# Performance work log

Measured on AMD Instinct MI355X. Metric: run time of the kernel, lower is better.

Reference implementation:

```python
import jax, jax.numpy as jnp
import numpy as np

EPS = 1e-9

def dice(x, alpha):
    # Dice: batch-norm over dim 0 (unbiased var, ddof=1), then gated blend.
    mu = jnp.mean(x, axis=0)
    var = jnp.var(x, axis=0, ddof=1)
    p = jax.nn.sigmoid((x - mu) / jnp.sqrt(var + EPS))
    return alpha * x * (1.0 - p) + x * p


def setup_inputs() -> dict:
    key = jax.random.key(0)
    ks = jax.random.split(key, 8)
    bs, seq, dim = 2048, 200, 64
    d_in = dim * 4
    return {
        "query": jax.random.normal(ks[0], (bs, dim), jnp.float32),
        "user_behavior": jax.random.normal(ks[1], (bs, seq, dim), jnp.float32),
        "mask": jax.random.uniform(ks[2], (bs, seq, 1), jnp.float32),
        "W1": jax.random.normal(ks[3], (d_in, 32), jnp.float32) / np.sqrt(d_in),
        "b1": jnp.zeros((32,), jnp.float32),
        "alpha1": jnp.zeros((1,), jnp.float32),
        "W2": jax.random.normal(ks[4], (32, 16), jnp.float32) / np.sqrt(32.0),
        "b2": jnp.zeros((16,), jnp.float32),
        "alpha2": jnp.zeros((1,), jnp.float32),
        "W3": jax.random.normal(ks[5], (16, 1), jnp.float32) / np.sqrt(16.0),
        "b3": jnp.zeros((1,), jnp.float32),
    }


def reference(query, user_behavior, mask, W1, b1, alpha1, W2, b2, alpha2, W3, b3):
    # query: (bs, dim) -> broadcast to (bs, seq, dim)
    q = jnp.broadcast_to(query[:, None, :], user_behavior.shape)
    attn_input = jnp.concatenate(
        [q, user_behavior, q - user_behavior, q * user_behavior], axis=-1
    )  # (bs, seq, 4*dim)
    h = dice(attn_input @ W1 + b1, alpha1)
    h = dice(h @ W2 + b2, alpha2)
    attns = h @ W3 + b3  # (bs, seq, 1)
    attns = attns * mask
    output = jnp.sum(user_behavior * attns, axis=1)  # (bs, dim)
    return output, attns
```

## Files before the change

### kernel.cpp

```cpp
#include <hip/hip_runtime.h>
#include <math.h>

#define BS  2048
#define SEQ 200
#define DIM 64
#define C1  32
#define C2  16
#define PAD 68

__device__ __forceinline__ float dice1(float x, float m, float r, float al) {
    float t = (x - m) * r;
    float p = 1.f / (1.f + __expf(-t));
    return x * (al + p * (1.f - al));
}

__global__ __launch_bounds__(256) void k_gemm1(const float* __restrict__ q,
                                               const float* __restrict__ ub,
                                               const float* __restrict__ W1,
                                               const float* __restrict__ b1,
                                               float* __restrict__ z1) {
    const int bs = blockIdx.x;
    const int tid = threadIdx.x;
    __shared__ __align__(16) float s_ub[SEQ * PAD];
    __shared__ __align__(16) float s_wc[DIM * C1];
    __shared__ __align__(16) float s_qw[C1];

    float4* s_ub4 = (float4*)s_ub;
    const float4* s_wc4 = (const float4*)s_wc;
    const float* qrow = q + bs * DIM;
    const float* ub_b = ub + (size_t)bs * SEQ * DIM;

    const float4* src4 = (const float4*)ub_b;
    for (int t = tid; t < SEQ * 16; t += 256)
        s_ub4[(t >> 4) * 17 + (t & 15)] = src4[t];

    const float4* w1b4 = (const float4*)(W1 + DIM * C1);
    const float4* w1c4 = (const float4*)(W1 + 2 * DIM * C1);
    const float4* w1d4 = (const float4*)(W1 + 3 * DIM * C1);
    for (int i4 = tid; i4 < DIM * C1 / 4; i4 += 256) {
        int d = i4 >> 3;
        float qd = qrow[d];
        float4 bb = w1b4[i4], cc = w1c4[i4], dd = w1d4[i4];
        float4 r;
        r.x = bb.x - cc.x + qd * dd.x;
        r.y = bb.y - cc.y + qd * dd.y;
        r.z = bb.z - cc.z + qd * dd.z;
        r.w = bb.w - cc.w + qd * dd.w;
        ((float4*)s_wc)[i4] = r;
    }
    if (tid < C1) {
        float a = b1[tid];
        #pragma unroll 8
        for (int d = 0; d < DIM; ++d)
            a = fmaf(qrow[d], W1[(d << 5) + tid] + W1[2 * DIM * C1 + (d << 5) + tid], a);
        s_qw[tid] = a;
    }
    __syncthreads();

    const int sl = tid >> 3;
    const int cq = tid & 7;
    const float4 qw = ((const float4*)s_qw)[cq];
    const float* su[7];
    float4 acc[7];
    #pragma unroll
    for (int i = 0; i < 7; ++i) {
        int r = sl + 32 * i;
        if (r > SEQ - 1) r = SEQ - 1;
        su[i] = s_ub + r * PAD;
        acc[i] = qw;
    }
    #pragma unroll 4
    for (int d = 0; d < DIM; ++d) {
        float4 w = s_wc4[(d << 3) + cq];
        #pragma unroll
        for (int i = 0; i < 7; ++i) {
            float u = su[i][d];
            acc[i].x = fmaf(u, w.x, acc[i].x);
            acc[i].y = fmaf(u, w.y, acc[i].y);
            acc[i].z = fmaf(u, w.z, acc[i].z);
            acc[i].w = fmaf(u, w.w, acc[i].w);
        }
    }
    float* z1_b = z1 + (size_t)bs * SEQ * C1;
    #pragma unroll
    for (int i = 0; i < 7; ++i) {
        int s = sl + 32 * i;
        if (s < SEQ) ((float4*)(z1_b + s * C1))[cq] = acc[i];
    }
}

template <int C>
__global__ __launch_bounds__(1024) void k_red(const float* __restrict__ z,
                                              float* __restrict__ mu,
                                              float* __restrict__ rstd) {
    constexpr int Q = C / 4;
    constexpr int NG = 1024 / Q;
    const int seq = blockIdx.x;
    const int cq = threadIdx.x % Q;
    const int g = threadIdx.x / Q;
    float4 s = {0.f, 0.f, 0.f, 0.f}, ss = {0.f, 0.f, 0.f, 0.f};
    for (int b = g; b < BS; b += NG) {
        float4 v = *(const float4*)(z + ((size_t)b * SEQ + seq) * C + cq * 4);
        s.x += v.x; s.y += v.y; s.z += v.z; s.w += v.w;
        ss.x = fmaf(v.x, v.x, ss.x);
        ss.y = fmaf(v.y, v.y, ss.y);
        ss.z = fmaf(v.z, v.z, ss.z);
        ss.w = fmaf(v.w, v.w, ss.w);
    }
    __shared__ __align__(16) float4 sh_s[1024];
    __shared__ __align__(16) float4 sh_ss[1024];
    sh_s[threadIdx.x] = s;
    sh_ss[threadIdx.x] = ss;
    for (int h = NG / 2; h > 0; h >>= 1) {
        __syncthreads();
        if (g < h) {
            int o = threadIdx.x + h * Q;
            float4 s2 = sh_s[o], ss2 = sh_ss[o];
            s.x += s2.x; s.y += s2.y; s.z += s2.z; s.w += s2.w;
            ss.x += ss2.x; ss.y += ss2.y; ss.z += ss2.z; ss.w += ss2.w;
            sh_s[threadIdx.x] = s;
            sh_ss[threadIdx.x] = ss;
        }
    }
    if (g == 0) {
        const float inv_n = 1.f / (float)BS;
        const float inv_n1 = 1.f / (float)(BS - 1);
        float4 m, r;
        m.x = s.x * inv_n; m.y = s.y * inv_n; m.z = s.z * inv_n; m.w = s.w * inv_n;
        r.x = rsqrtf((ss.x - s.x * m.x) * inv_n1 + 1e-9f);
        r.y = rsqrtf((ss.y - s.y * m.y) * inv_n1 + 1e-9f);
        r.z = rsqrtf((ss.z - s.z * m.z) * inv_n1 + 1e-9f);
        r.w = rsqrtf((ss.w - s.w * m.w) * inv_n1 + 1e-9f);
        *(float4*)(mu + seq * C + cq * 4) = m;
        *(float4*)(rstd + seq * C + cq * 4) = r;
    }
}

__global__ __launch_bounds__(256) void k_gemm2(const float* __restrict__ z1,
                                               const float* __restrict__ mu1,
                                               const float* __restrict__ rstd1,
                                               const float* __restrict__ alpha1,
                                               const float* __restrict__ W2,
                                               const float* __restrict__ b2,
                                               float* __restrict__ z2) {
    const int bs = blockIdx.x;
    const int tid = threadIdx.x;
    __shared__ __align__(16) float s_w2[C1 * C2];
    __shared__ float s_b2[C2];
    for (int i = tid; i < C1 * C2; i += 256) s_w2[i] = W2[i];
    if (tid < C2) s_b2[tid] = b2[tid];
    __syncthreads();
    if (tid >= SEQ) return;
    const float al = alpha1[0];
    const int seq = tid;
    const float4* z4 = (const float4*)(z1 + ((size_t)bs * SEQ + seq) * C1);
    const float4* m4 = (const float4*)(mu1 + seq * C1);
    const float4* r4 = (const float4*)(rstd1 + seq * C1);
    float h[C1];
    #pragma unroll
    for (int k = 0; k < C1 / 4; ++k) {
        float4 x = z4[k], m = m4[k], r = r4[k];
        h[k * 4 + 0] = dice1(x.x, m.x, r.x, al);
        h[k * 4 + 1] = dice1(x.y, m.y, r.y, al);
        h[k * 4 + 2] = dice1(x.z, m.z, r.z, al);
        h[k * 4 + 3] = dice1(x.w, m.w, r.w, al);
    }
    const float4* w4 = (const float4*)s_w2;
    float4 o[4];
    #pragma unroll
    for (int qd = 0; qd < 4; ++qd) {
        o[qd].x = s_b2[qd * 4 + 0];
        o[qd].y = s_b2[qd * 4 + 1];
        o[qd].z = s_b2[qd * 4 + 2];
        o[qd].w = s_b2[qd * 4 + 3];
    }
    #pragma unroll
    for (int c = 0; c < C1; ++c) {
        float hc = h[c];
        #pragma unroll
        for (int qd = 0; qd < 4; ++qd) {
            float4 w = w4[c * 4 + qd];
            o[qd].x = fmaf(hc, w.x, o[qd].x);
            o[qd].y = fmaf(hc, w.y, o[qd].y);
            o[qd].z = fmaf(hc, w.z, o[qd].z);
            o[qd].w = fmaf(hc, w.w, o[qd].w);
        }
    }
    float4* outp = (float4*)(z2 + ((size_t)bs * SEQ + seq) * C2);
    #pragma unroll
    for (int qd = 0; qd < 4; ++qd) outp[qd] = o[qd];
}

__global__ __launch_bounds__(256) void k_final(const float* __restrict__ z2,
                                               const float* __restrict__ mu2,
                                               const float* __restrict__ rstd2,
                                               const float* __restrict__ alpha2,
                                               const float* __restrict__ W3,
                                               const float* __restrict__ b3,
                                               const float* __restrict__ mask,
                                               const float* __restrict__ ub,
                                               float* __restrict__ out,
                                               float* __restrict__ attns) {
    const int bs = blockIdx.x;
    const int tid = threadIdx.x;
    __shared__ float s_attn[SEQ];
    __shared__ float s_w3[C2];
    __shared__ float s_part[4][DIM];
    if (tid < C2) s_w3[tid] = W3[tid];
    __syncthreads();
    if (tid < SEQ) {
        const float al = alpha2[0];
        const float bb3 = b3[0];
        const int seq = tid;
        const float4* z4 = (const float4*)(z2 + ((size_t)bs * SEQ + seq) * C2);
        const float4* m4 = (const float4*)(mu2 + seq * C2);
        const float4* r4 = (const float4*)(rstd2 + seq * C2);
        float a = bb3;
        #pragma unroll
        for (int k = 0; k < C2 / 4; ++k) {
            float4 x = z4[k], m = m4[k], r = r4[k];
            a = fmaf(dice1(x.x, m.x, r.x, al), s_w3[k * 4 + 0], a);
            a = fmaf(dice1(x.y, m.y, r.y, al), s_w3[k * 4 + 1], a);
            a = fmaf(dice1(x.z, m.z, r.z, al), s_w3[k * 4 + 2], a);
            a = fmaf(dice1(x.w, m.w, r.w, al), s_w3[k * 4 + 3], a);
        }
        a *= mask[bs * SEQ + seq];
        s_attn[seq] = a;
        attns[(size_t)bs * SEQ + seq] = a;
    }
    __syncthreads();
    const int d = tid & 63;
    const int sg = tid >> 6;
    float acc = 0.f;
    const float* ub_b = ub + (size_t)bs * SEQ * DIM;
    for (int s = sg; s < SEQ; s += 4)
        acc = fmaf(ub_b[s * DIM + d], s_attn[s], acc);
    s_part[sg][d] = acc;
    __syncthreads();
    if (tid < DIM) {
        float r = s_part[0][tid] + s_part[1][tid] + s_part[2][tid] + s_part[3][tid];
        out[(size_t)bs * DIM + tid] = r;
    }
}

extern "C" void kernel_launch(void* const* d_in, const int* in_sizes, int n_in,
                              void* d_out, int out_size, void* d_ws, size_t ws_size,
                              hipStream_t stream) {
    const float* q    = (const float*)d_in[0];
    const float* ub   = (const float*)d_in[1];
    const float* mask = (const float*)d_in[2];
    const float* W1   = (const float*)d_in[3];
    const float* b1   = (const float*)d_in[4];
    const float* a1   = (const float*)d_in[5];
    const float* W2   = (const float*)d_in[6];
    const float* b2   = (const float*)d_in[7];
    const float* a2   = (const float*)d_in[8];
    const float* W3   = (const float*)d_in[9];
    const float* b3   = (const float*)d_in[10];

    float* out   = (float*)d_out;
    float* attns = out + (size_t)BS * DIM;

    float* ws = (float*)d_ws;
    float* z1 = ws;
    float* z2 = z1 + (size_t)BS * SEQ * C1;
    float* mu1   = z2 + (size_t)BS * SEQ * C2;
    float* rstd1 = mu1 + SEQ * C1;
    float* mu2   = rstd1 + SEQ * C1;
    float* rstd2 = mu2 + SEQ * C2;

    hipLaunchKernelGGL(k_gemm1, dim3(BS), dim3(256), 0, stream, q, ub, W1, b1, z1);
    hipLaunchKernelGGL((k_red<C1>), dim3(SEQ), dim3(1024), 0, stream, z1, mu1, rstd1);
    hipLaunchKernelGGL(k_gemm2, dim3(BS), dim3(256), 0, stream, z1, mu1, rstd1, a1, W2, b2, z2);
    hipLaunchKernelGGL((k_red<C2>), dim3(SEQ), dim3(1024), 0, stream, z2, mu2, rstd2);
    hipLaunchKernelGGL(k_final, dim3(BS), dim3(256), 0, stream, z2, mu2, rstd2, a2, W3, b3, mask, ub, out, attns);
}
```

Baseline: 297.1 us.

## Use bf16 MFMA for first GEMM, split BN reductions, flatten gemm2 and vectorize pooling

The first projection now converts user_behavior and the folded weights to bf16 in swizzled shared memory and runs it with 16x16x32 bf16 MFMA instructions instead of scalar FMAs. The batch-norm reductions are split into a partial kernel over 8 batch chunks plus a small finalize kernel, which gives more parallelism than one 1024-thread block per sequence position. gemm2 drops its idle threads by flattening over all rows, and the final weighted pooling uses float4 loads with a tree reduction. The bf16 inputs reduce precision of z1, and the partial sums temporarily reuse the attns output buffer as scratch.

```diff
diff --git a/kernel.cpp b/kernel.cpp
--- a/kernel.cpp
+++ b/kernel.cpp
@@ -6,12 +6,22 @@
 #define DIM 64
 #define C1  32
 #define C2  16
-#define PAD 68
+
+typedef __attribute__((ext_vector_type(8))) short bf16x8_t;
+typedef __attribute__((ext_vector_type(4))) float f32x4_t;
+typedef __attribute__((ext_vector_type(4))) short short4_t;
 
 __device__ __forceinline__ float dice1(float x, float m, float r, float al) {
     float t = (x - m) * r;
     float p = 1.f / (1.f + __expf(-t));
     return x * (al + p * (1.f - al));
+}
+
+__device__ __forceinline__ unsigned short f2bf(float f) {
+    union { float f; unsigned u; } a;
+    a.f = f;
+    unsigned r = a.u + 0x7fff + ((a.u >> 16) & 1);
+    return (unsigned short)(r >> 16);
 }
 
 __global__ __launch_bounds__(256) void k_gemm1(const float* __restrict__ q,
@@ -21,85 +31,106 @@
                                                float* __restrict__ z1) {
     const int bs = blockIdx.x;
     const int tid = threadIdx.x;
-    __shared__ __align__(16) float s_ub[SEQ * PAD];
-    __shared__ __align__(16) float s_wc[DIM * C1];
+    __shared__ __align__(16) short s_A[208 * 64];
+    __shared__ __align__(16) short s_B[2 * 2 * 64 * 8];
     __shared__ __align__(16) float s_qw[C1];
 
-    float4* s_ub4 = (float4*)s_ub;
-    const float4* s_wc4 = (const float4*)s_wc;
+    char* sAc = (char*)s_A;
     const float* qrow = q + bs * DIM;
-    const float* ub_b = ub + (size_t)bs * SEQ * DIM;
-
-    const float4* src4 = (const float4*)ub_b;
-    for (int t = tid; t < SEQ * 16; t += 256)
-        s_ub4[(t >> 4) * 17 + (t & 15)] = src4[t];
-
-    const float4* w1b4 = (const float4*)(W1 + DIM * C1);
-    const float4* w1c4 = (const float4*)(W1 + 2 * DIM * C1);
-    const float4* w1d4 = (const float4*)(W1 + 3 * DIM * C1);
-    for (int i4 = tid; i4 < DIM * C1 / 4; i4 += 256) {
-        int d = i4 >> 3;
-        float qd = qrow[d];
-        float4 bb = w1b4[i4], cc = w1c4[i4], dd = w1d4[i4];
-        float4 r;
-        r.x = bb.x - cc.x + qd * dd.x;
-        r.y = bb.y - cc.y + qd * dd.y;
-        r.z = bb.z - cc.z + qd * dd.z;
-        r.w = bb.w - cc.w + qd * dd.w;
-        ((float4*)s_wc)[i4] = r;
+    const float4* src4 = (const float4*)(ub + (size_t)bs * SEQ * DIM);
+
+    float4 st[13];
+    #pragma unroll
+    for (int it = 0; it < 13; ++it) {
+        int i = tid + it * 256;
+        if (it < 12 || i < SEQ * 16) st[it] = src4[i];
+        else { st[it].x = 0.f; st[it].y = 0.f; st[it].z = 0.f; st[it].w = 0.f; }
+    }
+
+    {
+        const int kt = tid >> 7;
+        const int nt = (tid >> 6) & 1;
+        const int l  = tid & 63;
+        const int c  = nt * 16 + (l & 15);
+        bf16x8_t bfr;
+        #pragma unroll
+        for (int j = 0; j < 8; ++j) {
+            int k = kt * 32 + ((l >> 4) << 3) + j;
+            float wb = W1[(64 + k) * C1 + c] - W1[(128 + k) * C1 + c]
+                     + qrow[k] * W1[(192 + k) * C1 + c];
+            bfr[j] = (short)f2bf(wb);
+        }
+        *(bf16x8_t*)((char*)s_B + (((kt * 2 + nt) * 64) + l) * 16) = bfr;
     }
     if (tid < C1) {
         float a = b1[tid];
         #pragma unroll 8
         for (int d = 0; d < DIM; ++d)
-            a = fmaf(qrow[d], W1[(d << 5) + tid] + W1[2 * DIM * C1 + (d << 5) + tid], a);
+            a = fmaf(qrow[d], W1[d * C1 + tid] + W1[(128 + d) * C1 + tid], a);
         s_qw[tid] = a;
     }
+
+    #pragma unroll
+    for (int it = 0; it < 13; ++it) {
+        int i = tid + it * 256;
+        int row = i >> 4, f4 = i & 15;
+        int off = row * 128 + ((f4 * 8) ^ ((row & 7) << 4));
+        short4_t u;
+        u.x = (short)f2bf(st[it].x);
+        u.y = (short)f2bf(st[it].y);
+        u.z = (short)f2bf(st[it].z);
+        u.w = (short)f2bf(st[it].w);
+        *(short4_t*)(sAc + off) = u;
+    }
     __syncthreads();
 
-    const int sl = tid >> 3;
-    const int cq = tid & 7;
-    const float4 qw = ((const float4*)s_qw)[cq];
-    const float* su[7];
-    float4 acc[7];
-    #pragma unroll
-    for (int i = 0; i < 7; ++i) {
-        int r = sl + 32 * i;
-        if (r > SEQ - 1) r = SEQ - 1;
-        su[i] = s_ub + r * PAD;
-        acc[i] = qw;
-    }
-    #pragma unroll 4
-    for (int d = 0; d < DIM; ++d) {
-        float4 w = s_wc4[(d << 3) + cq];
+    const int wave = tid >> 6;
+    const int l = tid & 63;
+    const int g = l >> 4;
+    const bf16x8_t b00 = *(const bf16x8_t*)((char*)s_B + (0 * 64 + l) * 16);
+    const bf16x8_t b01 = *(const bf16x8_t*)((char*)s_B + (1 * 64 + l) * 16);
+    const bf16x8_t b10 = *(const bf16x8_t*)((char*)s_B + (2 * 64 + l) * 16);
+    const bf16x8_t b11 = *(const bf16x8_t*)((char*)s_B + (3 * 64 + l) * 16);
+    const float qw0 = s_qw[l & 15];
+    const float qw1 = s_qw[16 + (l & 15)];
+    float* z1_b = z1 + (size_t)bs * SEQ * C1;
+
+    for (int mt = wave; mt < 13; mt += 4) {
+        const int row = mt * 16 + (l & 15);
+        const int sw = (row & 7) << 4;
+        bf16x8_t a0 = *(const bf16x8_t*)(sAc + row * 128 + ((g * 16) ^ sw));
+        bf16x8_t a1 = *(const bf16x8_t*)(sAc + row * 128 + (((64 + g * 16)) ^ sw));
+        f32x4_t acc0 = {0.f, 0.f, 0.f, 0.f};
+        f32x4_t acc1 = {0.f, 0.f, 0.f, 0.f};
+        acc0 = __builtin_amdgcn_mfma_f32_16x16x32_bf16(a0, b00, acc0, 0, 0, 0);
+        acc0 = __builtin_amdgcn_mfma_f32_16x16x32_bf16(a1, b10, acc0, 0, 0, 0);
+        acc1 = __builtin_amdgcn_mfma_f32_16x16x32_bf16(a0, b01, acc1, 0, 0, 0);
+        acc1 = __builtin_amdgcn_mfma_f32_16x16x32_bf16(a1, b11, acc1, 0, 0, 0);
+        const int orow = mt * 16 + g * 4;
         #pragma unroll
-        for (int i = 0; i < 7; ++i) {
-            float u = su[i][d];
-            acc[i].x = fmaf(u, w.x, acc[i].x);
-            acc[i].y = fmaf(u, w.y, acc[i].y);
-            acc[i].z = fmaf(u, w.z, acc[i].z);
-            acc[i].w = fmaf(u, w.w, acc[i].w);
-        }
-    }
-    float* z1_b = z1 + (size_t)bs * SEQ * C1;
-    #pragma unroll
-    for (int i = 0; i < 7; ++i) {
-        int s = sl + 32 * i;
-        if (s < SEQ) ((float4*)(z1_b + s * C1))[cq] = acc[i];
+        for (int r = 0; r < 4; ++r) {
+            int rr = orow + r;
+            if (rr < SEQ) {
+                z1_b[rr * C1 + (l & 15)]      = acc0[r] + qw0;
+                z1_b[rr * C1 + 16 + (l & 15)] = acc1[r] + qw1;
+            }
+        }
     }
 }
 
 template <int C>
-__global__ __launch_bounds__(1024) void k_red(const float* __restrict__ z,
-                                              float* __restrict__ mu,
-                                              float* __restrict__ rstd) {
+__global__ __launch_bounds__(256) void k_redA(const float* __restrict__ z,
+                                              float* __restrict__ pS,
+                                              float* __restrict__ pQ) {
     constexpr int Q = C / 4;
-    constexpr int NG = 1024 / Q;
+    constexpr int NG = 256 / Q;
     const int seq = blockIdx.x;
+    const int part = blockIdx.y;
     const int cq = threadIdx.x % Q;
     const int g = threadIdx.x / Q;
     float4 s = {0.f, 0.f, 0.f, 0.f}, ss = {0.f, 0.f, 0.f, 0.f};
-    for (int b = g; b < BS; b += NG) {
+    const int b0 = part * 256;
+    for (int b = b0 + g; b < b0 + 256; b += NG) {
         float4 v = *(const float4*)(z + ((size_t)b * SEQ + seq) * C + cq * 4);
         s.x += v.x; s.y += v.y; s.z += v.z; s.w += v.w;
         ss.x = fmaf(v.x, v.x, ss.x);
@@ -107,33 +138,45 @@
         ss.z = fmaf(v.z, v.z, ss.z);
         ss.w = fmaf(v.w, v.w, ss.w);
     }
-    __shared__ __align__(16) float4 sh_s[1024];
-    __shared__ __align__(16) float4 sh_ss[1024];
+    __shared__ __align__(16) float4 sh_s[256];
+    __shared__ __align__(16) float4 sh_q[256];
     sh_s[threadIdx.x] = s;
-    sh_ss[threadIdx.x] = ss;
+    sh_q[threadIdx.x] = ss;
     for (int h = NG / 2; h > 0; h >>= 1) {
         __syncthreads();
         if (g < h) {
             int o = threadIdx.x + h * Q;
-            float4 s2 = sh_s[o], ss2 = sh_ss[o];
+            float4 s2 = sh_s[o], q2 = sh_q[o];
             s.x += s2.x; s.y += s2.y; s.z += s2.z; s.w += s2.w;
-            ss.x += ss2.x; ss.y += ss2.y; ss.z += ss2.z; ss.w += ss2.w;
+            ss.x += q2.x; ss.y += q2.y; ss.z += q2.z; ss.w += q2.w;
             sh_s[threadIdx.x] = s;
-            sh_ss[threadIdx.x] = ss;
+            sh_q[threadIdx.x] = ss;
         }
     }
     if (g == 0) {
-        const float inv_n = 1.f / (float)BS;
-        const float inv_n1 = 1.f / (float)(BS - 1);
-        float4 m, r;
-        m.x = s.x * inv_n; m.y = s.y * inv_n; m.z = s.z * inv_n; m.w = s.w * inv_n;
-        r.x = rsqrtf((ss.x - s.x * m.x) * inv_n1 + 1e-9f);
-        r.y = rsqrtf((ss.y - s.y * m.y) * inv_n1 + 1e-9f);
-        r.z = rsqrtf((ss.z - s.z * m.z) * inv_n1 + 1e-9f);
-        r.w = rsqrtf((ss.w - s.w * m.w) * inv_n1 + 1e-9f);
-        *(float4*)(mu + seq * C + cq * 4) = m;
-        *(float4*)(rstd + seq * C + cq * 4) = r;
-    }
+        *(float4*)(pS + ((size_t)part * SEQ + seq) * C + cq * 4) = s;
+        *(float4*)(pQ + ((size_t)part * SEQ + seq) * C + cq * 4) = ss;
+    }
+}
+
+template <int C>
+__global__ __launch_bounds__(64) void k_redB(const float* __restrict__ pS,
+                                             const float* __restrict__ pQ,
+                                             float* __restrict__ mu,
+                                             float* __restrict__ rstd) {
+    const int seq = blockIdx.x;
+    const int c = threadIdx.x;
+    if (c >= C) return;
+    float s = 0.f, ss = 0.f;
+    #pragma unroll
+    for (int p = 0; p < 8; ++p) {
+        s += pS[((size_t)p * SEQ + seq) * C + c];
+        ss += pQ[((size_t)p * SEQ + seq) * C + c];
+    }
+    float m = s / (float)BS;
+    float var = (ss - s * m) / (float)(BS - 1);
+    mu[seq * C + c] = m;
+    rstd[seq * C + c] = rsqrtf(var + 1e-9f);
 }
 
 __global__ __launch_bounds__(256) void k_gemm2(const float* __restrict__ z1,
@@ -143,17 +186,17 @@
                                                const float* __restrict__ W2,
                                                const float* __restrict__ b2,
                                                float* __restrict__ z2) {
-    const int bs = blockIdx.x;
     const int tid = threadIdx.x;
     __shared__ __align__(16) float s_w2[C1 * C2];
     __shared__ float s_b2[C2];
     for (int i = tid; i < C1 * C2; i += 256) s_w2[i] = W2[i];
     if (tid < C2) s_b2[tid] = b2[tid];
     __syncthreads();
-    if (tid >= SEQ) return;
+    const int gidx = blockIdx.x * 256 + tid;
+    const int bsb = gidx / SEQ;
+    const int seq = gidx - bsb * SEQ;
     const float al = alpha1[0];
-    const int seq = tid;
-    const float4* z4 = (const float4*)(z1 + ((size_t)bs * SEQ + seq) * C1);
+    const float4* z4 = (const float4*)(z1 + (size_t)gidx * C1);
     const float4* m4 = (const float4*)(mu1 + seq * C1);
     const float4* r4 = (const float4*)(rstd1 + seq * C1);
     float h[C1];
@@ -186,7 +229,7 @@
             o[qd].w = fmaf(hc, w.w, o[qd].w);
         }
     }
-    float4* outp = (float4*)(z2 + ((size_t)bs * SEQ + seq) * C2);
+    float4* outp = (float4*)(z2 + (size_t)gidx * C2);
     #pragma unroll
     for (int qd = 0; qd < 4; ++qd) outp[qd] = o[qd];
 }
@@ -205,16 +248,15 @@
     const int tid = threadIdx.x;
     __shared__ float s_attn[SEQ];
     __shared__ float s_w3[C2];
-    __shared__ float s_part[4][DIM];
+    __shared__ __align__(16) float4 s_pool[256];
     if (tid < C2) s_w3[tid] = W3[tid];
     __syncthreads();
     if (tid < SEQ) {
         const float al = alpha2[0];
         const float bb3 = b3[0];
-        const int seq = tid;
-        const float4* z4 = (const float4*)(z2 + ((size_t)bs * SEQ + seq) * C2);
-        const float4* m4 = (const float4*)(mu2 + seq * C2);
-        const float4* r4 = (const float4*)(rstd2 + seq * C2);
+        const float4* z4 = (const float4*)(z2 + ((size_t)bs * SEQ + tid) * C2);
+        const float4* m4 = (const float4*)(mu2 + tid * C2);
+        const float4* r4 = (const float4*)(rstd2 + tid * C2);
         float a = bb3;
         #pragma unroll
         for (int k = 0; k < C2 / 4; ++k) {
@@ -224,23 +266,34 @@
             a = fmaf(dice1(x.z, m.z, r.z, al), s_w3[k * 4 + 2], a);
             a = fmaf(dice1(x.w, m.w, r.w, al), s_w3[k * 4 + 3], a);
         }
-        a *= mask[bs * SEQ + seq];
-        s_attn[seq] = a;
-        attns[(size_t)bs * SEQ + seq] = a;
+        a *= mask[bs * SEQ + tid];
+        s_attn[tid] = a;
+        attns[(size_t)bs * SEQ + tid] = a;
     }
     __syncthreads();
-    const int d = tid & 63;
-    const int sg = tid >> 6;
-    float acc = 0.f;
-    const float* ub_b = ub + (size_t)bs * SEQ * DIM;
-    for (int s = sg; s < SEQ; s += 4)
-        acc = fmaf(ub_b[s * DIM + d], s_attn[s], acc);
-    s_part[sg][d] = acc;
-    __syncthreads();
-    if (tid < DIM) {
-        float r = s_part[0][tid] + s_part[1][tid] + s_part[2][tid] + s_part[3][tid];
-        out[(size_t)bs * DIM + tid] = r;
-    }
+    const int dq = tid & 15;
+    const int sg = tid >> 4;
+    float4 acc = {0.f, 0.f, 0.f, 0.f};
+    const float4* ub4 = (const float4*)(ub + (size_t)bs * SEQ * DIM);
+    for (int s = sg; s < SEQ; s += 16) {
+        float a = s_attn[s];
+        float4 v = ub4[s * 16 + dq];
+        acc.x = fmaf(v.x, a, acc.x);
+        acc.y = fmaf(v.y, a, acc.y);
+        acc.z = fmaf(v.z, a, acc.z);
+        acc.w = fmaf(v.w, a, acc.w);
+    }
+    s_pool[tid] = acc;
+    for (int h = 8; h > 0; h >>= 1) {
+        __syncthreads();
+        if (sg < h) {
+            float4 o = s_pool[tid + h * 16];
+            acc.x += o.x; acc.y += o.y; acc.z += o.z; acc.w += o.w;
+            s_pool[tid] = acc;
+        }
+    }
+    if (sg == 0)
+        *(float4*)(out + (size_t)bs * DIM + dq * 4) = acc;
 }
 
 extern "C" void kernel_launch(void* const* d_in, const int* in_sizes, int n_in,
@@ -268,10 +321,14 @@
     float* rstd1 = mu1 + SEQ * C1;
     float* mu2   = rstd1 + SEQ * C1;
     float* rstd2 = mu2 + SEQ * C2;
+    float* pS    = attns;
+    float* pQ    = pS + 8 * SEQ * C1;
 
     hipLaunchKernelGGL(k_gemm1, dim3(BS), dim3(256), 0, stream, q, ub, W1, b1, z1);
-    hipLaunchKernelGGL((k_red<C1>), dim3(SEQ), dim3(1024), 0, stream, z1, mu1, rstd1);
-    hipLaunchKernelGGL(k_gemm2, dim3(BS), dim3(256), 0, stream, z1, mu1, rstd1, a1, W2, b2, z2);
-    hipLaunchKernelGGL((k_red<C2>), dim3(SEQ), dim3(1024), 0, stream, z2, mu2, rstd2);
+    hipLaunchKernelGGL((k_redA<C1>), dim3(SEQ, 8), dim3(256), 0, stream, z1, pS, pQ);
+    hipLaunchKernelGGL((k_redB<C1>), dim3(SEQ), dim3(64), 0, stream, pS, pQ, mu1, rstd1);
+    hipLaunchKernelGGL(k_gemm2, dim3(BS * SEQ / 256), dim3(256), 0, stream, z1, mu1, rstd1, a1, W2, b2, z2);
+    hipLaunchKernelGGL((k_redA<C2>), dim3(SEQ, 8), dim3(256), 0, stream, z2, pS, pQ);
+    hipLaunchKernelGGL((k_redB<C2>), dim3(SEQ), dim3(64), 0, stream, pS, pQ, mu2, rstd2);
     hipLaunchKernelGGL(k_final, dim3(BS), dim3(256), 0, stream, z2, mu2, rstd2, a2, W3, b3, mask, ub, out, attns);
 }
```

New measurement: 272.7 us. -8.2%, faster.
